# Performance work log

Hardware: AMD Instinct MI355X
Metric: run time of the kernel (lower is better)

The kernel has to match this reference:

```python
import jax, jax.numpy as jnp
import numpy as np

H = 1024
E = 8
TOP_K = 2
B, S = 4, 2048


def setup_inputs() -> dict:
    key = jax.random.key(0)
    ks = jax.random.split(key, 8)
    scale = 0.02
    return {
        "x": jax.random.normal(ks[0], (B, S, H), dtype=jnp.float32),
        "router_w": jax.random.normal(ks[1], (H, E), dtype=jnp.float32) * scale,
        "router_b": jnp.zeros((E,), dtype=jnp.float32),
        "w1": jax.random.normal(ks[2], (E, H, 4 * H), dtype=jnp.float32) * scale,
        "b1": jnp.zeros((E, 4 * H), dtype=jnp.float32),
        "w2": jax.random.normal(ks[3], (E, 4 * H, H), dtype=jnp.float32) * scale,
        "b2": jnp.zeros((E, H), dtype=jnp.float32),
    }


def reference(x, router_w, router_b, w1, b1, w2, b2):
    b, s, h = x.shape
    n_exp = w1.shape[0]
    x_flat = x.reshape(-1, h)  # [T, H]
    T = x_flat.shape[0]

    # Router: softmax then top-k, renormalize top-k probs (matches torch code).
    logits = x_flat @ router_w + router_b            # [T, E]
    probs = jax.nn.softmax(logits, axis=-1)
    top_values, top_indices = jax.lax.top_k(probs, TOP_K)  # [T, k]
    top_values = top_values / jnp.sum(top_values, axis=-1, keepdims=True)

    # Per-token combine weight for each expert (0 if token not routed there).
    combine = jnp.zeros((T, n_exp), dtype=x.dtype)
    combine = combine.at[jnp.arange(T)[:, None], top_indices].add(top_values)  # [T, E]

    # Loop over the small fixed expert set; masked combine weights zero out
    # contributions from unrouted tokens, matching the gather/scatter original.
    out = jnp.zeros_like(x_flat)
    for e in range(n_exp):
        hmid = jax.nn.gelu(x_flat @ w1[e] + b1[e], approximate=False)  # [T, 4H]
        y = hmid @ w2[e] + b2[e]                                       # [T, H]
        out = out + combine[:, e:e + 1] * y
    return out.reshape(b, s, h)
```

## Files before the change

### kernel.cpp

```cpp
#include <hip/hip_runtime.h>
#include <hip/hip_bf16.h>
#include <math.h>

#define TT 8192
#define HD 1024
#define FHD 4096
#define NE 8
#define NTMAX 136

typedef short s16x8 __attribute__((ext_vector_type(8)));
typedef float f32x4 __attribute__((ext_vector_type(4)));
using bf16 = __hip_bfloat16;
typedef unsigned int u32;

#define OFF_COUNTS 0
#define OFF_CURSOR 64
#define OFF_OFFS   128
#define OFF_E0     256
#define OFF_E1     (OFF_E0 + 4*TT)
#define OFF_W0     (OFF_E1 + 4*TT)
#define OFF_W1     (OFF_W0 + 4*TT)
#define OFF_S0     (OFF_W1 + 4*TT)
#define OFF_S1     (OFF_S0 + 4*TT)
#define OFF_TID    (OFF_S1 + 4*TT)
#define OFF_TW     (OFF_TID + 8*TT)
#define OFF_TMR    (OFF_TW + 8*TT)
#define OFF_TME    (OFF_TMR + 4*144)
#define OFF_TMN    (OFF_TME + 4*144)
#define OFF_XBF    (OFF_TMN + 64)
#define OFF_W1T    (OFF_XBF + 2*TT*HD)
#define OFF_W2T    (OFF_W1T + 2*NE*HD*FHD)
#define OFF_HMID   (OFF_W2T + 2*NE*HD*FHD)
#define OFF_YS     (OFF_HMID + (size_t)2*(2*TT)*FHD)

#define BM 128
#define BN 128
#define BK 32

__device__ __forceinline__ void gload_lds16(const void* g, void* l) {
    __builtin_amdgcn_global_load_lds(
        (const __attribute__((address_space(1))) u32*)g,
        (__attribute__((address_space(3))) u32*)l, 16, 0, 0);
}

__global__ __launch_bounds__(256) void cast_x_kernel(const float* __restrict__ x, bf16* __restrict__ xbf) {
    int i = (blockIdx.x * 256 + threadIdx.x) * 8;
    float4 a = *reinterpret_cast<const float4*>(&x[i]);
    float4 b = *reinterpret_cast<const float4*>(&x[i + 4]);
    bf16 h[8];
    h[0] = __float2bfloat16(a.x); h[1] = __float2bfloat16(a.y);
    h[2] = __float2bfloat16(a.z); h[3] = __float2bfloat16(a.w);
    h[4] = __float2bfloat16(b.x); h[5] = __float2bfloat16(b.y);
    h[6] = __float2bfloat16(b.z); h[7] = __float2bfloat16(b.w);
    *reinterpret_cast<uint4*>(&xbf[i]) = *reinterpret_cast<uint4*>(h);
}

__global__ __launch_bounds__(256) void transpose_cast_kernel(const float* __restrict__ in,
        bf16* __restrict__ out, int R, int C) {
    __shared__ float tile[64][65];
    int rt = R >> 6, ct = C >> 6;
    int e = blockIdx.x / (rt * ct);
    int rem = blockIdx.x % (rt * ct);
    int r0 = (rem / ct) << 6, c0 = (rem % ct) << 6;
    const float* ine = in + (size_t)e * R * C;
    bf16* oute = out + (size_t)e * R * C;
    int tid = threadIdx.x;
#pragma unroll
    for (int i = 0; i < 4; ++i) {
        int lin = tid + i * 256;
        int r = lin >> 4, cg = lin & 15;
        float4 v = *reinterpret_cast<const float4*>(&ine[(size_t)(r0 + r) * C + c0 + cg * 4]);
        tile[r][cg * 4 + 0] = v.x; tile[r][cg * 4 + 1] = v.y;
        tile[r][cg * 4 + 2] = v.z; tile[r][cg * 4 + 3] = v.w;
    }
    __syncthreads();
#pragma unroll
    for (int i = 0; i < 4; ++i) {
        int lin = tid + i * 256;
        int n = lin >> 4, kg = lin & 15;
        bf16 h[4];
        h[0] = __float2bfloat16(tile[kg * 4 + 0][n]);
        h[1] = __float2bfloat16(tile[kg * 4 + 1][n]);
        h[2] = __float2bfloat16(tile[kg * 4 + 2][n]);
        h[3] = __float2bfloat16(tile[kg * 4 + 3][n]);
        *reinterpret_cast<uint2*>(&oute[(size_t)(c0 + n) * R + r0 + kg * 4]) =
            *reinterpret_cast<uint2*>(h);
    }
}

__global__ __launch_bounds__(256) void router_kernel(const float* __restrict__ x,
        const float* __restrict__ rw, const float* __restrict__ rb,
        int* __restrict__ e0a, int* __restrict__ e1a,
        float* __restrict__ w0a, float* __restrict__ w1a, int* __restrict__ counts) {
    int wid = threadIdx.x >> 6, lane = threadIdx.x & 63;
    int t = blockIdx.x * 4 + wid;
    const float* xp = x + (size_t)t * HD + lane * 16;
    float xv[16];
#pragma unroll
    for (int j = 0; j < 4; ++j) {
        float4 v = *reinterpret_cast<const float4*>(&xp[j * 4]);
        xv[4 * j] = v.x; xv[4 * j + 1] = v.y; xv[4 * j + 2] = v.z; xv[4 * j + 3] = v.w;
    }
    float acc[8] = {0.f, 0.f, 0.f, 0.f, 0.f, 0.f, 0.f, 0.f};
    const float* rp = rw + (size_t)(lane * 16) * NE;
#pragma unroll
    for (int hh = 0; hh < 16; ++hh) {
        float4 r0 = *reinterpret_cast<const float4*>(&rp[hh * 8]);
        float4 r1 = *reinterpret_cast<const float4*>(&rp[hh * 8 + 4]);
        acc[0] += xv[hh] * r0.x; acc[1] += xv[hh] * r0.y;
        acc[2] += xv[hh] * r0.z; acc[3] += xv[hh] * r0.w;
        acc[4] += xv[hh] * r1.x; acc[5] += xv[hh] * r1.y;
        acc[6] += xv[hh] * r1.z; acc[7] += xv[hh] * r1.w;
    }
#pragma unroll
    for (int e = 0; e < 8; ++e) {
#pragma unroll
        for (int off = 32; off > 0; off >>= 1) acc[e] += __shfl_xor(acc[e], off, 64);
    }
    if (lane == 0) {
        float lg[8];
#pragma unroll
        for (int e = 0; e < 8; ++e) lg[e] = acc[e] + rb[e];
        int a = 0;
#pragma unroll
        for (int e = 1; e < 8; ++e) if (lg[e] > lg[a]) a = e;
        int b = (a == 0) ? 1 : 0;
#pragma unroll
        for (int e = 0; e < 8; ++e) if (e != a && e != b && lg[e] > lg[b]) b = e;
        float wa = 1.0f / (1.0f + expf(lg[b] - lg[a]));
        float wb = 1.0f / (1.0f + expf(lg[a] - lg[b]));
        e0a[t] = a; e1a[t] = b; w0a[t] = wa; w1a[t] = wb;
        atomicAdd(&counts[a], 1);
        atomicAdd(&counts[b], 1);
    }
}

__global__ void scan_offsets_kernel(const int* __restrict__ counts, int* __restrict__ offs,
        int* __restrict__ cursor, int* __restrict__ tmr, int* __restrict__ tme,
        int* __restrict__ tmn) {
    if (threadIdx.x == 0 && blockIdx.x == 0) {
        int s = 0, nt = 0;
        for (int e = 0; e < NE; ++e) {
            offs[e] = s; cursor[e] = s;
            int c = counts[e];
            for (int j = 0; j < c; j += BM) { tmr[nt] = s + j; tme[nt] = e; ++nt; }
            s += c;
        }
        offs[NE] = s;
        tmn[0] = nt;
        for (int i = nt; i < NTMAX; ++i) { tmr[i] = 0; tme[i] = 0; }
    }
}

__global__ __launch_bounds__(256) void scatter_kernel(const int* __restrict__ e0a, const int* __restrict__ e1a,
        const float* __restrict__ w0a, const float* __restrict__ w1a,
        int* __restrict__ cursor, int* __restrict__ tid_arr, float* __restrict__ tw_arr,
        int* __restrict__ slot0, int* __restrict__ slot1) {
    int t = blockIdx.x * 256 + threadIdx.x;
    int s0 = atomicAdd(&cursor[e0a[t]], 1);
    tid_arr[s0] = t; tw_arr[s0] = w0a[t]; slot0[t] = s0;
    int s1 = atomicAdd(&cursor[e1a[t]], 1);
    tid_arr[s1] = t; tw_arr[s1] = w1a[t]; slot1[t] = s1;
}

__global__ __launch_bounds__(256) void gemm1_kernel(const bf16* __restrict__ xbf, const bf16* __restrict__ w1t,
        const float* __restrict__ b1, const int* __restrict__ offs,
        const int* __restrict__ tid_arr, bf16* __restrict__ hmid,
        const int* __restrict__ tmr, const int* __restrict__ tme, const int* __restrict__ tmn) {
    __shared__ bf16 As[BM * BK];
    __shared__ bf16 Bs[BN * BK];
    __shared__ int toks[BM];
    int nwg = gridDim.x;
    int orig = blockIdx.x;
    int wg = (orig & 7) * (nwg >> 3) + (orig >> 3);
    int nt = wg / NTMAX;
    int tidx = wg % NTMAX;
    if (tidx >= tmn[0]) return;
    int e = tme[tidx];
    int row0 = tmr[tidx];
    int s1 = offs[e + 1];
    int n0 = nt * BN;
    int tid = threadIdx.x;
    if (tid < BM) { int s = row0 + tid; toks[tid] = tid_arr[(s < s1) ? s : (s1 - 1)]; }
    __syncthreads();
    int lane = tid & 63, w = tid >> 6;
    int wrow = (w >> 1) * 64, wcol = (w & 1) * 64;
    int lr = lane & 15, lk = (lane >> 4) * 8;
    int srow = lane >> 2, seg = lane & 3;
    int tokA0 = toks[w * 32 + srow];
    int tokA1 = toks[w * 32 + 16 + srow];
    const bf16* w1e = w1t + (size_t)e * FHD * HD;
    const bf16* bsrc0 = w1e + (size_t)(n0 + w * 32 + srow) * HD + seg * 8;
    const bf16* bsrc1 = w1e + (size_t)(n0 + w * 32 + 16 + srow) * HD + seg * 8;
    const bf16* asrc0 = xbf + (size_t)tokA0 * HD + seg * 8;
    const bf16* asrc1 = xbf + (size_t)tokA1 * HD + seg * 8;
    bf16* aDst0 = &As[(w * 32) * BK];
    bf16* aDst1 = &As[(w * 32 + 16) * BK];
    bf16* bDst0 = &Bs[(w * 32) * BK];
    bf16* bDst1 = &Bs[(w * 32 + 16) * BK];
    f32x4 acc[4][4] = {};
    for (int k0 = 0; k0 < HD; k0 += BK) {
        gload_lds16(asrc0 + k0, aDst0);
        gload_lds16(asrc1 + k0, aDst1);
        gload_lds16(bsrc0 + k0, bDst0);
        gload_lds16(bsrc1 + k0, bDst1);
        __syncthreads();
        s16x8 aF[4], bF[4];
#pragma unroll
        for (int m = 0; m < 4; ++m) aF[m] = *reinterpret_cast<const s16x8*>(&As[(wrow + m * 16 + lr) * BK + lk]);
#pragma unroll
        for (int n = 0; n < 4; ++n) bF[n] = *reinterpret_cast<const s16x8*>(&Bs[(wcol + n * 16 + lr) * BK + lk]);
#pragma unroll
        for (int m = 0; m < 4; ++m)
#pragma unroll
            for (int n = 0; n < 4; ++n)
                acc[m][n] = __builtin_amdgcn_mfma_f32_16x16x32_bf16(aF[m], bF[n], acc[m][n], 0, 0, 0);
        __syncthreads();
    }
#pragma unroll
    for (int m = 0; m < 4; ++m) {
#pragma unroll
        for (int n = 0; n < 4; ++n) {
            int col = n0 + wcol + n * 16 + lr;
            float bv = b1[(size_t)e * FHD + col];
#pragma unroll
            for (int r = 0; r < 4; ++r) {
                int row = wrow + m * 16 + (lane >> 4) * 4 + r;
                int slot = row0 + row;
                if (slot < s1) {
                    float v2 = acc[m][n][r] + bv;
                    v2 = 0.5f * v2 * (1.0f + erff(v2 * 0.70710678118f));
                    hmid[(size_t)slot * FHD + col] = __float2bfloat16(v2);
                }
            }
        }
    }
}

__global__ __launch_bounds__(256) void gemm2_kernel(const bf16* __restrict__ hmid, const bf16* __restrict__ w2t,
        const float* __restrict__ b2, const int* __restrict__ offs, float* __restrict__ ys,
        const int* __restrict__ tmr, const int* __restrict__ tme, const int* __restrict__ tmn) {
    __shared__ bf16 As[BM * BK];
    __shared__ bf16 Bs[BN * BK];
    int nwg = gridDim.x;
    int orig = blockIdx.x;
    int wg = (orig & 7) * (nwg >> 3) + (orig >> 3);
    int nt = wg / NTMAX;
    int tidx = wg % NTMAX;
    if (tidx >= tmn[0]) return;
    int e = tme[tidx];
    int row0 = tmr[tidx];
    int s1 = offs[e + 1];
    int n0 = nt * BN;
    int tid = threadIdx.x;
    int lane = tid & 63, w = tid >> 6;
    int wrow = (w >> 1) * 64, wcol = (w & 1) * 64;
    int lr = lane & 15, lk = (lane >> 4) * 8;
    int srow = lane >> 2, seg = lane & 3;
    int ar0 = row0 + w * 32 + srow;      if (ar0 >= s1) ar0 = s1 - 1;
    int ar1 = row0 + w * 32 + 16 + srow; if (ar1 >= s1) ar1 = s1 - 1;
    const bf16* w2e = w2t + (size_t)e * HD * FHD;
    const bf16* bsrc0 = w2e + (size_t)(n0 + w * 32 + srow) * FHD + seg * 8;
    const bf16* bsrc1 = w2e + (size_t)(n0 + w * 32 + 16 + srow) * FHD + seg * 8;
    const bf16* asrc0 = hmid + (size_t)ar0 * FHD + seg * 8;
    const bf16* asrc1 = hmid + (size_t)ar1 * FHD + seg * 8;
    bf16* aDst0 = &As[(w * 32) * BK];
    bf16* aDst1 = &As[(w * 32 + 16) * BK];
    bf16* bDst0 = &Bs[(w * 32) * BK];
    bf16* bDst1 = &Bs[(w * 32 + 16) * BK];
    f32x4 acc[4][4] = {};
    for (int k0 = 0; k0 < FHD; k0 += BK) {
        gload_lds16(asrc0 + k0, aDst0);
        gload_lds16(asrc1 + k0, aDst1);
        gload_lds16(bsrc0 + k0, bDst0);
        gload_lds16(bsrc1 + k0, bDst1);
        __syncthreads();
        s16x8 aF[4], bF[4];
#pragma unroll
        for (int m = 0; m < 4; ++m) aF[m] = *reinterpret_cast<const s16x8*>(&As[(wrow + m * 16 + lr) * BK + lk]);
#pragma unroll
        for (int n = 0; n < 4; ++n) bF[n] = *reinterpret_cast<const s16x8*>(&Bs[(wcol + n * 16 + lr) * BK + lk]);
#pragma unroll
        for (int m = 0; m < 4; ++m)
#pragma unroll
            for (int n = 0; n < 4; ++n)
                acc[m][n] = __builtin_amdgcn_mfma_f32_16x16x32_bf16(aF[m], bF[n], acc[m][n], 0, 0, 0);
        __syncthreads();
    }
#pragma unroll
    for (int m = 0; m < 4; ++m) {
#pragma unroll
        for (int n = 0; n < 4; ++n) {
            int col = n0 + wcol + n * 16 + lr;
            float bv = b2[(size_t)e * HD + col];
#pragma unroll
            for (int r = 0; r < 4; ++r) {
                int row = wrow + m * 16 + (lane >> 4) * 4 + r;
                int slot = row0 + row;
                if (slot < s1) ys[(size_t)slot * HD + col] = acc[m][n][r] + bv;
            }
        }
    }
}

__global__ __launch_bounds__(256) void combine_kernel(const float* __restrict__ ys,
        const int* __restrict__ slot0, const int* __restrict__ slot1,
        const float* __restrict__ tw, float* __restrict__ out) {
    int t = blockIdx.x;
    int c = threadIdx.x * 4;
    int sa = slot0[t], sb = slot1[t];
    float wa = tw[sa], wb = tw[sb];
    float4 a = *reinterpret_cast<const float4*>(&ys[(size_t)sa * HD + c]);
    float4 b = *reinterpret_cast<const float4*>(&ys[(size_t)sb * HD + c]);
    float4 o;
    o.x = wa * a.x + wb * b.x; o.y = wa * a.y + wb * b.y;
    o.z = wa * a.z + wb * b.z; o.w = wa * a.w + wb * b.w;
    *reinterpret_cast<float4*>(&out[(size_t)t * HD + c]) = o;
}

extern "C" void kernel_launch(void* const* d_in, const int* in_sizes, int n_in,
                              void* d_out, int out_size, void* d_ws, size_t ws_size,
                              hipStream_t stream) {
    const float* x  = (const float*)d_in[0];
    const float* rw = (const float*)d_in[1];
    const float* rb = (const float*)d_in[2];
    const float* w1 = (const float*)d_in[3];
    const float* b1 = (const float*)d_in[4];
    const float* w2 = (const float*)d_in[5];
    const float* b2 = (const float*)d_in[6];
    float* out = (float*)d_out;
    char* ws = (char*)d_ws;

    int*   counts  = (int*)(ws + OFF_COUNTS);
    int*   cursor  = (int*)(ws + OFF_CURSOR);
    int*   offs    = (int*)(ws + OFF_OFFS);
    int*   e0a     = (int*)(ws + OFF_E0);
    int*   e1a     = (int*)(ws + OFF_E1);
    float* w0a     = (float*)(ws + OFF_W0);
    float* w1a     = (float*)(ws + OFF_W1);
    int*   slot0   = (int*)(ws + OFF_S0);
    int*   slot1   = (int*)(ws + OFF_S1);
    int*   tid_arr = (int*)(ws + OFF_TID);
    float* tw_arr  = (float*)(ws + OFF_TW);
    int*   tmr     = (int*)(ws + OFF_TMR);
    int*   tme     = (int*)(ws + OFF_TME);
    int*   tmn     = (int*)(ws + OFF_TMN);
    bf16*  xbf     = (bf16*)(ws + OFF_XBF);
    bf16*  w1t     = (bf16*)(ws + OFF_W1T);
    bf16*  w2t     = (bf16*)(ws + OFF_W2T);
    bf16*  hmid    = (bf16*)(ws + OFF_HMID);
    float* ys      = (float*)(ws + OFF_YS);

    hipMemsetAsync(counts, 0, 64, stream);

    cast_x_kernel<<<TT * HD / 2048, 256, 0, stream>>>(x, xbf);
    transpose_cast_kernel<<<NE * (HD / 64) * (FHD / 64), 256, 0, stream>>>(w1, w1t, HD, FHD);
    transpose_cast_kernel<<<NE * (FHD / 64) * (HD / 64), 256, 0, stream>>>(w2, w2t, FHD, HD);
    router_kernel<<<TT / 4, 256, 0, stream>>>(x, rw, rb, e0a, e1a, w0a, w1a, counts);
    scan_offsets_kernel<<<1, 64, 0, stream>>>(counts, offs, cursor, tmr, tme, tmn);
    scatter_kernel<<<TT / 256, 256, 0, stream>>>(e0a, e1a, w0a, w1a, cursor, tid_arr, tw_arr, slot0, slot1);
    gemm1_kernel<<<(FHD / BN) * NTMAX, 256, 0, stream>>>(xbf, w1t, b1, offs, tid_arr, hmid, tmr, tme, tmn);
    gemm2_kernel<<<(HD / BN) * NTMAX, 256, 0, stream>>>(hmid, w2t, b2, offs, ys, tmr, tme, tmn);
    combine_kernel<<<TT, 256, 0, stream>>>(ys, slot0, slot1, tw_arr, out);
}
```

Baseline: 929.2 us.

## Enlarge MoE GEMM tiles, add 4-stage LDS pipeline with swizzled layout

Both expert GEMMs move to 512-thread blocks with 256-row token tiles (256x256 tiles for gemm1, 256x128 for gemm2). The single-buffered LDS loop with two syncthreads per k-step becomes a 4-deep ring buffer that prefetches 3 k-tiles ahead and uses partial vmcnt waits. An XOR swizzle on LDS rows is meant to avoid bank conflicts, and s_setprio is raised around the MFMA block. This targets global-load latency and barrier stalls at the cost of much larger LDS use (128KB in gemm1), lower occupancy, and more padded rows per expert tile.

```diff
diff --git a/kernel.cpp b/kernel.cpp
--- a/kernel.cpp
+++ b/kernel.cpp
@@ -6,7 +6,7 @@
 #define HD 1024
 #define FHD 4096
 #define NE 8
-#define NTMAX 136
+#define TMAX 72
 
 typedef short s16x8 __attribute__((ext_vector_type(8)));
 typedef float f32x4 __attribute__((ext_vector_type(4)));
@@ -33,10 +33,6 @@
 #define OFF_HMID   (OFF_W2T + 2*NE*HD*FHD)
 #define OFF_YS     (OFF_HMID + (size_t)2*(2*TT)*FHD)
 
-#define BM 128
-#define BN 128
-#define BK 32
-
 __device__ __forceinline__ void gload_lds16(const void* g, void* l) {
     __builtin_amdgcn_global_load_lds(
         (const __attribute__((address_space(1))) u32*)g,
@@ -143,12 +139,12 @@
         for (int e = 0; e < NE; ++e) {
             offs[e] = s; cursor[e] = s;
             int c = counts[e];
-            for (int j = 0; j < c; j += BM) { tmr[nt] = s + j; tme[nt] = e; ++nt; }
+            for (int j = 0; j < c; j += 256) { tmr[nt] = s + j; tme[nt] = e; ++nt; }
             s += c;
         }
         offs[NE] = s;
         tmn[0] = nt;
-        for (int i = nt; i < NTMAX; ++i) { tmr[i] = 0; tme[i] = 0; }
+        for (int i = nt; i < TMAX; ++i) { tmr[i] = 0; tme[i] = 0; }
     }
 }
 
@@ -163,69 +159,87 @@
     tid_arr[s1] = t; tw_arr[s1] = w1a[t]; slot1[t] = s1;
 }
 
-__global__ __launch_bounds__(256) void gemm1_kernel(const bf16* __restrict__ xbf, const bf16* __restrict__ w1t,
+__global__ __launch_bounds__(512) void gemm1_kernel(const bf16* __restrict__ xbf, const bf16* __restrict__ w1t,
         const float* __restrict__ b1, const int* __restrict__ offs,
         const int* __restrict__ tid_arr, bf16* __restrict__ hmid,
         const int* __restrict__ tmr, const int* __restrict__ tme, const int* __restrict__ tmn) {
-    __shared__ bf16 As[BM * BK];
-    __shared__ bf16 Bs[BN * BK];
-    __shared__ int toks[BM];
+    __shared__ bf16 As[4 * 256 * 32];
+    __shared__ bf16 Bs[4 * 256 * 32];
+    __shared__ int toks[256];
     int nwg = gridDim.x;
     int orig = blockIdx.x;
     int wg = (orig & 7) * (nwg >> 3) + (orig >> 3);
-    int nt = wg / NTMAX;
-    int tidx = wg % NTMAX;
+    int nt = wg / TMAX, tidx = wg % TMAX;
     if (tidx >= tmn[0]) return;
-    int e = tme[tidx];
-    int row0 = tmr[tidx];
-    int s1 = offs[e + 1];
-    int n0 = nt * BN;
-    int tid = threadIdx.x;
-    if (tid < BM) { int s = row0 + tid; toks[tid] = tid_arr[(s < s1) ? s : (s1 - 1)]; }
+    int e = tme[tidx], row0 = tmr[tidx], s1 = offs[e + 1];
+    int n0 = nt * 256;
+    int t = threadIdx.x;
+    if (t < 256) { int s = row0 + t; toks[t] = tid_arr[(s < s1) ? s : (s1 - 1)]; }
     __syncthreads();
-    int lane = tid & 63, w = tid >> 6;
-    int wrow = (w >> 1) * 64, wcol = (w & 1) * 64;
+    int lane = t & 63, w = t >> 6;
+    const bf16* w1e = w1t + (size_t)e * FHD * HD;
+    int rs = t >> 2, g = t & 3;
+    int swz = (g ^ ((rs >> 1) & 3)) * 8;
+    const bf16* srcA0 = xbf + (size_t)toks[rs] * HD + swz;
+    const bf16* srcA1 = xbf + (size_t)toks[rs + 128] * HD + swz;
+    const bf16* srcB0 = w1e + (size_t)(n0 + rs) * HD + swz;
+    const bf16* srcB1 = w1e + (size_t)(n0 + rs + 128) * HD + swz;
+    int dst0 = w * 512;
+    int dst1 = 4096 + w * 512;
+    int wr = w >> 2, wc = w & 3;
     int lr = lane & 15, lk = (lane >> 4) * 8;
-    int srow = lane >> 2, seg = lane & 3;
-    int tokA0 = toks[w * 32 + srow];
-    int tokA1 = toks[w * 32 + 16 + srow];
-    const bf16* w1e = w1t + (size_t)e * FHD * HD;
-    const bf16* bsrc0 = w1e + (size_t)(n0 + w * 32 + srow) * HD + seg * 8;
-    const bf16* bsrc1 = w1e + (size_t)(n0 + w * 32 + 16 + srow) * HD + seg * 8;
-    const bf16* asrc0 = xbf + (size_t)tokA0 * HD + seg * 8;
-    const bf16* asrc1 = xbf + (size_t)tokA1 * HD + seg * 8;
-    bf16* aDst0 = &As[(w * 32) * BK];
-    bf16* aDst1 = &As[(w * 32 + 16) * BK];
-    bf16* bDst0 = &Bs[(w * 32) * BK];
-    bf16* bDst1 = &Bs[(w * 32 + 16) * BK];
-    f32x4 acc[4][4] = {};
-    for (int k0 = 0; k0 < HD; k0 += BK) {
-        gload_lds16(asrc0 + k0, aDst0);
-        gload_lds16(asrc1 + k0, aDst1);
-        gload_lds16(bsrc0 + k0, bDst0);
-        gload_lds16(bsrc1 + k0, bDst1);
-        __syncthreads();
-        s16x8 aF[4], bF[4];
-#pragma unroll
-        for (int m = 0; m < 4; ++m) aF[m] = *reinterpret_cast<const s16x8*>(&As[(wrow + m * 16 + lr) * BK + lk]);
-#pragma unroll
-        for (int n = 0; n < 4; ++n) bF[n] = *reinterpret_cast<const s16x8*>(&Bs[(wcol + n * 16 + lr) * BK + lk]);
-#pragma unroll
-        for (int m = 0; m < 4; ++m)
+    int offA[8], offB[4];
+#pragma unroll
+    for (int m = 0; m < 8; ++m) { int row = wr * 128 + m * 16 + lr; offA[m] = row * 32 + (lk ^ (8 * ((row >> 1) & 3))); }
+#pragma unroll
+    for (int n = 0; n < 4; ++n) { int row = wc * 64 + n * 16 + lr; offB[n] = row * 32 + (lk ^ (8 * ((row >> 1) & 3))); }
+    f32x4 acc[8][4] = {};
+#pragma unroll
+    for (int kt = 0; kt < 3; ++kt) {
+        int bo = kt * 8192, ko = kt * 32;
+        gload_lds16(srcA0 + ko, &As[bo + dst0]);
+        gload_lds16(srcA1 + ko, &As[bo + dst1]);
+        gload_lds16(srcB0 + ko, &Bs[bo + dst0]);
+        gload_lds16(srcB1 + ko, &Bs[bo + dst1]);
+    }
+    asm volatile("s_waitcnt vmcnt(8)" ::: "memory");
+    __builtin_amdgcn_s_barrier();
+    for (int kt = 0; kt < HD / 32; ++kt) {
+        const bf16* Ab = &As[(kt & 3) * 8192];
+        const bf16* Bb = &Bs[(kt & 3) * 8192];
+        s16x8 aF[8], bF[4];
+#pragma unroll
+        for (int m = 0; m < 8; ++m) aF[m] = *reinterpret_cast<const s16x8*>(&Ab[offA[m]]);
+#pragma unroll
+        for (int n = 0; n < 4; ++n) bF[n] = *reinterpret_cast<const s16x8*>(&Bb[offB[n]]);
+        int kt3 = kt + 3; if (kt3 >= HD / 32) kt3 -= HD / 32;
+        int bo = (kt3 & 3) * 8192, ko = kt3 * 32;
+        gload_lds16(srcA0 + ko, &As[bo + dst0]);
+        gload_lds16(srcA1 + ko, &As[bo + dst1]);
+        gload_lds16(srcB0 + ko, &Bs[bo + dst0]);
+        gload_lds16(srcB1 + ko, &Bs[bo + dst1]);
+        asm volatile("s_waitcnt vmcnt(8)" ::: "memory");
+        __builtin_amdgcn_s_barrier();
+        __builtin_amdgcn_sched_barrier(0);
+        __builtin_amdgcn_s_setprio(1);
+#pragma unroll
+        for (int m = 0; m < 8; ++m)
 #pragma unroll
             for (int n = 0; n < 4; ++n)
                 acc[m][n] = __builtin_amdgcn_mfma_f32_16x16x32_bf16(aF[m], bF[n], acc[m][n], 0, 0, 0);
-        __syncthreads();
-    }
-#pragma unroll
-    for (int m = 0; m < 4; ++m) {
-#pragma unroll
-        for (int n = 0; n < 4; ++n) {
-            int col = n0 + wcol + n * 16 + lr;
-            float bv = b1[(size_t)e * FHD + col];
+        __builtin_amdgcn_s_setprio(0);
+        __builtin_amdgcn_sched_barrier(0);
+        __builtin_amdgcn_s_barrier();
+    }
+#pragma unroll
+    for (int n = 0; n < 4; ++n) {
+        int col = n0 + wc * 64 + n * 16 + lr;
+        float bv = b1[(size_t)e * FHD + col];
+#pragma unroll
+        for (int m = 0; m < 8; ++m) {
 #pragma unroll
             for (int r = 0; r < 4; ++r) {
-                int row = wrow + m * 16 + (lane >> 4) * 4 + r;
+                int row = wr * 128 + m * 16 + (lane >> 4) * 4 + r;
                 int slot = row0 + row;
                 if (slot < s1) {
                     float v2 = acc[m][n][r] + bv;
@@ -237,65 +251,83 @@
     }
 }
 
-__global__ __launch_bounds__(256) void gemm2_kernel(const bf16* __restrict__ hmid, const bf16* __restrict__ w2t,
+__global__ __launch_bounds__(512) void gemm2_kernel(const bf16* __restrict__ hmid, const bf16* __restrict__ w2t,
         const float* __restrict__ b2, const int* __restrict__ offs, float* __restrict__ ys,
         const int* __restrict__ tmr, const int* __restrict__ tme, const int* __restrict__ tmn) {
-    __shared__ bf16 As[BM * BK];
-    __shared__ bf16 Bs[BN * BK];
+    __shared__ bf16 As[4 * 256 * 32];
+    __shared__ bf16 Bs[4 * 128 * 32];
     int nwg = gridDim.x;
     int orig = blockIdx.x;
     int wg = (orig & 7) * (nwg >> 3) + (orig >> 3);
-    int nt = wg / NTMAX;
-    int tidx = wg % NTMAX;
+    int nt = wg / TMAX, tidx = wg % TMAX;
     if (tidx >= tmn[0]) return;
-    int e = tme[tidx];
-    int row0 = tmr[tidx];
-    int s1 = offs[e + 1];
-    int n0 = nt * BN;
-    int tid = threadIdx.x;
-    int lane = tid & 63, w = tid >> 6;
-    int wrow = (w >> 1) * 64, wcol = (w & 1) * 64;
+    int e = tme[tidx], row0 = tmr[tidx], s1 = offs[e + 1];
+    int n0 = nt * 128;
+    int t = threadIdx.x;
+    int lane = t & 63, w = t >> 6;
+    const bf16* w2e = w2t + (size_t)e * HD * FHD;
+    int rs = t >> 2, g = t & 3;
+    int swz = (g ^ ((rs >> 1) & 3)) * 8;
+    int ar0 = row0 + rs;       if (ar0 >= s1) ar0 = s1 - 1;
+    int ar1 = row0 + rs + 128; if (ar1 >= s1) ar1 = s1 - 1;
+    const bf16* srcA0 = hmid + (size_t)ar0 * FHD + swz;
+    const bf16* srcA1 = hmid + (size_t)ar1 * FHD + swz;
+    const bf16* srcB0 = w2e + (size_t)(n0 + rs) * FHD + swz;
+    int dstA0 = w * 512;
+    int dstA1 = 4096 + w * 512;
+    int dstB  = w * 512;
+    int wr = w >> 1, wc = w & 1;
     int lr = lane & 15, lk = (lane >> 4) * 8;
-    int srow = lane >> 2, seg = lane & 3;
-    int ar0 = row0 + w * 32 + srow;      if (ar0 >= s1) ar0 = s1 - 1;
-    int ar1 = row0 + w * 32 + 16 + srow; if (ar1 >= s1) ar1 = s1 - 1;
-    const bf16* w2e = w2t + (size_t)e * HD * FHD;
-    const bf16* bsrc0 = w2e + (size_t)(n0 + w * 32 + srow) * FHD + seg * 8;
-    const bf16* bsrc1 = w2e + (size_t)(n0 + w * 32 + 16 + srow) * FHD + seg * 8;
-    const bf16* asrc0 = hmid + (size_t)ar0 * FHD + seg * 8;
-    const bf16* asrc1 = hmid + (size_t)ar1 * FHD + seg * 8;
-    bf16* aDst0 = &As[(w * 32) * BK];
-    bf16* aDst1 = &As[(w * 32 + 16) * BK];
-    bf16* bDst0 = &Bs[(w * 32) * BK];
-    bf16* bDst1 = &Bs[(w * 32 + 16) * BK];
+    int offA[4], offB[4];
+#pragma unroll
+    for (int m = 0; m < 4; ++m) { int row = wr * 64 + m * 16 + lr; offA[m] = row * 32 + (lk ^ (8 * ((row >> 1) & 3))); }
+#pragma unroll
+    for (int n = 0; n < 4; ++n) { int row = wc * 64 + n * 16 + lr; offB[n] = row * 32 + (lk ^ (8 * ((row >> 1) & 3))); }
     f32x4 acc[4][4] = {};
-    for (int k0 = 0; k0 < FHD; k0 += BK) {
-        gload_lds16(asrc0 + k0, aDst0);
-        gload_lds16(asrc1 + k0, aDst1);
-        gload_lds16(bsrc0 + k0, bDst0);
-        gload_lds16(bsrc1 + k0, bDst1);
-        __syncthreads();
+#pragma unroll
+    for (int kt = 0; kt < 3; ++kt) {
+        int boA = kt * 8192, boB = kt * 4096, ko = kt * 32;
+        gload_lds16(srcA0 + ko, &As[boA + dstA0]);
+        gload_lds16(srcA1 + ko, &As[boA + dstA1]);
+        gload_lds16(srcB0 + ko, &Bs[boB + dstB]);
+    }
+    asm volatile("s_waitcnt vmcnt(6)" ::: "memory");
+    __builtin_amdgcn_s_barrier();
+    for (int kt = 0; kt < FHD / 32; ++kt) {
+        const bf16* Ab = &As[(kt & 3) * 8192];
+        const bf16* Bb = &Bs[(kt & 3) * 4096];
         s16x8 aF[4], bF[4];
 #pragma unroll
-        for (int m = 0; m < 4; ++m) aF[m] = *reinterpret_cast<const s16x8*>(&As[(wrow + m * 16 + lr) * BK + lk]);
-#pragma unroll
-        for (int n = 0; n < 4; ++n) bF[n] = *reinterpret_cast<const s16x8*>(&Bs[(wcol + n * 16 + lr) * BK + lk]);
+        for (int m = 0; m < 4; ++m) aF[m] = *reinterpret_cast<const s16x8*>(&Ab[offA[m]]);
+#pragma unroll
+        for (int n = 0; n < 4; ++n) bF[n] = *reinterpret_cast<const s16x8*>(&Bb[offB[n]]);
+        int kt3 = kt + 3; if (kt3 >= FHD / 32) kt3 -= FHD / 32;
+        int boA = (kt3 & 3) * 8192, boB = (kt3 & 3) * 4096, ko = kt3 * 32;
+        gload_lds16(srcA0 + ko, &As[boA + dstA0]);
+        gload_lds16(srcA1 + ko, &As[boA + dstA1]);
+        gload_lds16(srcB0 + ko, &Bs[boB + dstB]);
+        asm volatile("s_waitcnt vmcnt(6)" ::: "memory");
+        __builtin_amdgcn_s_barrier();
+        __builtin_amdgcn_sched_barrier(0);
+        __builtin_amdgcn_s_setprio(1);
 #pragma unroll
         for (int m = 0; m < 4; ++m)
 #pragma unroll
             for (int n = 0; n < 4; ++n)
                 acc[m][n] = __builtin_amdgcn_mfma_f32_16x16x32_bf16(aF[m], bF[n], acc[m][n], 0, 0, 0);
-        __syncthreads();
-    }
-#pragma unroll
-    for (int m = 0; m < 4; ++m) {
-#pragma unroll
-        for (int n = 0; n < 4; ++n) {
-            int col = n0 + wcol + n * 16 + lr;
-            float bv = b2[(size_t)e * HD + col];
+        __builtin_amdgcn_s_setprio(0);
+        __builtin_amdgcn_sched_barrier(0);
+        __builtin_amdgcn_s_barrier();
+    }
+#pragma unroll
+    for (int n = 0; n < 4; ++n) {
+        int col = n0 + wc * 64 + n * 16 + lr;
+        float bv = b2[(size_t)e * HD + col];
+#pragma unroll
+        for (int m = 0; m < 4; ++m) {
 #pragma unroll
             for (int r = 0; r < 4; ++r) {
-                int row = wrow + m * 16 + (lane >> 4) * 4 + r;
+                int row = wr * 64 + m * 16 + (lane >> 4) * 4 + r;
                 int slot = row0 + row;
                 if (slot < s1) ys[(size_t)slot * HD + col] = acc[m][n][r] + bv;
             }
@@ -359,7 +391,7 @@
     router_kernel<<<TT / 4, 256, 0, stream>>>(x, rw, rb, e0a, e1a, w0a, w1a, counts);
     scan_offsets_kernel<<<1, 64, 0, stream>>>(counts, offs, cursor, tmr, tme, tmn);
     scatter_kernel<<<TT / 256, 256, 0, stream>>>(e0a, e1a, w0a, w1a, cursor, tid_arr, tw_arr, slot0, slot1);
-    gemm1_kernel<<<(FHD / BN) * NTMAX, 256, 0, stream>>>(xbf, w1t, b1, offs, tid_arr, hmid, tmr, tme, tmn);
-    gemm2_kernel<<<(HD / BN) * NTMAX, 256, 0, stream>>>(hmid, w2t, b2, offs, ys, tmr, tme, tmn);
+    gemm1_kernel<<<(FHD / 256) * TMAX, 512, 0, stream>>>(xbf, w1t, b1, offs, tid_arr, hmid, tmr, tme, tmn);
+    gemm2_kernel<<<(HD / 128) * TMAX, 512, 0, stream>>>(hmid, w2t, b2, offs, ys, tmr, tme, tmn);
     combine_kernel<<<TT, 256, 0, stream>>>(ys, slot0, slot1, tw_arr, out);
 }
```

After: 968.9 us. 1.04x slower.

## Widen GEMM K-tile to 64 with swizzled LDS and fuse combine via atomics

Applied to the files above, without the earlier changes.

Both expert GEMMs now load 64-wide K tiles into XOR-swizzled shared memory, which halves the number of barriers per K and is meant to avoid LDS bank conflicts. They also raise MFMA issue priority and set launch bounds for occupancy. The second GEMM applies the routing weight and atomically adds into the zeroed output, which removes the fp32 intermediate buffer and the separate combine kernel. In exchange, the fp32 atomics make the summation order nondeterministic and add atomic traffic to the output.

```diff
diff --git a/kernel.cpp b/kernel.cpp
--- a/kernel.cpp
+++ b/kernel.cpp
@@ -31,11 +31,6 @@
 #define OFF_W1T    (OFF_XBF + 2*TT*HD)
 #define OFF_W2T    (OFF_W1T + 2*NE*HD*FHD)
 #define OFF_HMID   (OFF_W2T + 2*NE*HD*FHD)
-#define OFF_YS     (OFF_HMID + (size_t)2*(2*TT)*FHD)
-
-#define BM 128
-#define BN 128
-#define BK 32
 
 __device__ __forceinline__ void gload_lds16(const void* g, void* l) {
     __builtin_amdgcn_global_load_lds(
@@ -143,7 +138,7 @@
         for (int e = 0; e < NE; ++e) {
             offs[e] = s; cursor[e] = s;
             int c = counts[e];
-            for (int j = 0; j < c; j += BM) { tmr[nt] = s + j; tme[nt] = e; ++nt; }
+            for (int j = 0; j < c; j += 128) { tmr[nt] = s + j; tme[nt] = e; ++nt; }
             s += c;
         }
         offs[NE] = s;
@@ -154,78 +149,94 @@
 
 __global__ __launch_bounds__(256) void scatter_kernel(const int* __restrict__ e0a, const int* __restrict__ e1a,
         const float* __restrict__ w0a, const float* __restrict__ w1a,
-        int* __restrict__ cursor, int* __restrict__ tid_arr, float* __restrict__ tw_arr,
-        int* __restrict__ slot0, int* __restrict__ slot1) {
+        int* __restrict__ cursor, int* __restrict__ tid_arr, float* __restrict__ tw_arr) {
     int t = blockIdx.x * 256 + threadIdx.x;
     int s0 = atomicAdd(&cursor[e0a[t]], 1);
-    tid_arr[s0] = t; tw_arr[s0] = w0a[t]; slot0[t] = s0;
+    tid_arr[s0] = t; tw_arr[s0] = w0a[t];
     int s1 = atomicAdd(&cursor[e1a[t]], 1);
-    tid_arr[s1] = t; tw_arr[s1] = w1a[t]; slot1[t] = s1;
-}
-
-__global__ __launch_bounds__(256) void gemm1_kernel(const bf16* __restrict__ xbf, const bf16* __restrict__ w1t,
-        const float* __restrict__ b1, const int* __restrict__ offs,
-        const int* __restrict__ tid_arr, bf16* __restrict__ hmid,
-        const int* __restrict__ tmr, const int* __restrict__ tme, const int* __restrict__ tmn) {
-    __shared__ bf16 As[BM * BK];
-    __shared__ bf16 Bs[BN * BK];
-    __shared__ int toks[BM];
+    tid_arr[s1] = t; tw_arr[s1] = w1a[t];
+}
+
+__global__ __launch_bounds__(256, 4) void gemm1_kernel(const bf16* __restrict__ xbf,
+        const bf16* __restrict__ w1t, const float* __restrict__ b1,
+        const int* __restrict__ offs, const int* __restrict__ tid_arr,
+        bf16* __restrict__ hmid, const int* __restrict__ tmr,
+        const int* __restrict__ tme, const int* __restrict__ tmn) {
+    __shared__ bf16 As[128 * 64];
+    __shared__ bf16 Bs[128 * 64];
+    __shared__ int toks[128];
     int nwg = gridDim.x;
     int orig = blockIdx.x;
     int wg = (orig & 7) * (nwg >> 3) + (orig >> 3);
-    int nt = wg / NTMAX;
-    int tidx = wg % NTMAX;
+    int nt = wg / NTMAX, tidx = wg % NTMAX;
     if (tidx >= tmn[0]) return;
-    int e = tme[tidx];
-    int row0 = tmr[tidx];
-    int s1 = offs[e + 1];
-    int n0 = nt * BN;
-    int tid = threadIdx.x;
-    if (tid < BM) { int s = row0 + tid; toks[tid] = tid_arr[(s < s1) ? s : (s1 - 1)]; }
+    int e = tme[tidx], row0 = tmr[tidx], s1 = offs[e + 1];
+    int n0 = nt * 128;
+    int t = threadIdx.x;
+    if (t < 128) { int s = row0 + t; toks[t] = tid_arr[(s < s1) ? s : (s1 - 1)]; }
     __syncthreads();
-    int lane = tid & 63, w = tid >> 6;
-    int wrow = (w >> 1) * 64, wcol = (w & 1) * 64;
-    int lr = lane & 15, lk = (lane >> 4) * 8;
-    int srow = lane >> 2, seg = lane & 3;
-    int tokA0 = toks[w * 32 + srow];
-    int tokA1 = toks[w * 32 + 16 + srow];
+    int lane = t & 63, w = t >> 6;
+    int wr = w >> 1, wc = w & 1;
+    int lr = lane & 15, kg = lane >> 4;
+    int srow = t >> 3, soct = t & 7;
+    int socts = (soct ^ (srow & 7)) * 8;
     const bf16* w1e = w1t + (size_t)e * FHD * HD;
-    const bf16* bsrc0 = w1e + (size_t)(n0 + w * 32 + srow) * HD + seg * 8;
-    const bf16* bsrc1 = w1e + (size_t)(n0 + w * 32 + 16 + srow) * HD + seg * 8;
-    const bf16* asrc0 = xbf + (size_t)tokA0 * HD + seg * 8;
-    const bf16* asrc1 = xbf + (size_t)tokA1 * HD + seg * 8;
-    bf16* aDst0 = &As[(w * 32) * BK];
-    bf16* aDst1 = &As[(w * 32 + 16) * BK];
-    bf16* bDst0 = &Bs[(w * 32) * BK];
-    bf16* bDst1 = &Bs[(w * 32 + 16) * BK];
+    const bf16* pA[4]; const bf16* pB[4];
+#pragma unroll
+    for (int i = 0; i < 4; ++i) {
+        int r = i * 32 + srow;
+        pA[i] = xbf + (size_t)toks[r] * HD + socts;
+        pB[i] = w1e + (size_t)(n0 + r) * HD + socts;
+    }
+    int ldst = t * 8;
+    int offA[4][2], offB[4][2];
+#pragma unroll
+    for (int m = 0; m < 4; ++m) {
+        int rowA = wr * 64 + m * 16 + lr;
+        int rowB = wc * 64 + m * 16 + lr;
+#pragma unroll
+        for (int ks = 0; ks < 2; ++ks) {
+            offA[m][ks] = rowA * 64 + ((ks * 32 + kg * 8) ^ ((lr & 7) << 3));
+            offB[m][ks] = rowB * 64 + ((ks * 32 + kg * 8) ^ ((lr & 7) << 3));
+        }
+    }
     f32x4 acc[4][4] = {};
-    for (int k0 = 0; k0 < HD; k0 += BK) {
-        gload_lds16(asrc0 + k0, aDst0);
-        gload_lds16(asrc1 + k0, aDst1);
-        gload_lds16(bsrc0 + k0, bDst0);
-        gload_lds16(bsrc1 + k0, bDst1);
+    for (int kt = 0; kt < HD / 64; ++kt) {
+        int ko = kt * 64;
+#pragma unroll
+        for (int i = 0; i < 4; ++i) {
+            gload_lds16(pA[i] + ko, &As[i * 2048 + ldst]);
+            gload_lds16(pB[i] + ko, &Bs[i * 2048 + ldst]);
+        }
         __syncthreads();
-        s16x8 aF[4], bF[4];
-#pragma unroll
-        for (int m = 0; m < 4; ++m) aF[m] = *reinterpret_cast<const s16x8*>(&As[(wrow + m * 16 + lr) * BK + lk]);
-#pragma unroll
-        for (int n = 0; n < 4; ++n) bF[n] = *reinterpret_cast<const s16x8*>(&Bs[(wcol + n * 16 + lr) * BK + lk]);
+        s16x8 af[4][2], bfr[4][2];
 #pragma unroll
         for (int m = 0; m < 4; ++m)
 #pragma unroll
+            for (int ks = 0; ks < 2; ++ks) {
+                af[m][ks] = *reinterpret_cast<const s16x8*>(&As[offA[m][ks]]);
+                bfr[m][ks] = *reinterpret_cast<const s16x8*>(&Bs[offB[m][ks]]);
+            }
+        __builtin_amdgcn_s_setprio(1);
+#pragma unroll
+        for (int m = 0; m < 4; ++m)
+#pragma unroll
             for (int n = 0; n < 4; ++n)
-                acc[m][n] = __builtin_amdgcn_mfma_f32_16x16x32_bf16(aF[m], bF[n], acc[m][n], 0, 0, 0);
+#pragma unroll
+                for (int ks = 0; ks < 2; ++ks)
+                    acc[m][n] = __builtin_amdgcn_mfma_f32_16x16x32_bf16(af[m][ks], bfr[n][ks], acc[m][n], 0, 0, 0);
+        __builtin_amdgcn_s_setprio(0);
         __syncthreads();
     }
 #pragma unroll
     for (int m = 0; m < 4; ++m) {
 #pragma unroll
         for (int n = 0; n < 4; ++n) {
-            int col = n0 + wcol + n * 16 + lr;
+            int col = n0 + wc * 64 + n * 16 + lr;
             float bv = b1[(size_t)e * FHD + col];
 #pragma unroll
             for (int r = 0; r < 4; ++r) {
-                int row = wrow + m * 16 + (lane >> 4) * 4 + r;
+                int row = wr * 64 + m * 16 + kg * 4 + r;
                 int slot = row0 + row;
                 if (slot < s1) {
                     float v2 = acc[m][n][r] + bv;
@@ -237,85 +248,101 @@
     }
 }
 
-__global__ __launch_bounds__(256) void gemm2_kernel(const bf16* __restrict__ hmid, const bf16* __restrict__ w2t,
-        const float* __restrict__ b2, const int* __restrict__ offs, float* __restrict__ ys,
+__global__ __launch_bounds__(256, 4) void gemm2_kernel(const bf16* __restrict__ hmid,
+        const bf16* __restrict__ w2t, const float* __restrict__ b2,
+        const int* __restrict__ offs, const int* __restrict__ tid_arr,
+        const float* __restrict__ tw_arr, float* __restrict__ out,
         const int* __restrict__ tmr, const int* __restrict__ tme, const int* __restrict__ tmn) {
-    __shared__ bf16 As[BM * BK];
-    __shared__ bf16 Bs[BN * BK];
+    __shared__ bf16 As[128 * 64];
+    __shared__ bf16 Bs[128 * 64];
+    __shared__ int toks[128];
+    __shared__ float tws[128];
     int nwg = gridDim.x;
     int orig = blockIdx.x;
     int wg = (orig & 7) * (nwg >> 3) + (orig >> 3);
-    int nt = wg / NTMAX;
-    int tidx = wg % NTMAX;
+    int nt = wg / NTMAX, tidx = wg % NTMAX;
     if (tidx >= tmn[0]) return;
-    int e = tme[tidx];
-    int row0 = tmr[tidx];
-    int s1 = offs[e + 1];
-    int n0 = nt * BN;
-    int tid = threadIdx.x;
-    int lane = tid & 63, w = tid >> 6;
-    int wrow = (w >> 1) * 64, wcol = (w & 1) * 64;
-    int lr = lane & 15, lk = (lane >> 4) * 8;
-    int srow = lane >> 2, seg = lane & 3;
-    int ar0 = row0 + w * 32 + srow;      if (ar0 >= s1) ar0 = s1 - 1;
-    int ar1 = row0 + w * 32 + 16 + srow; if (ar1 >= s1) ar1 = s1 - 1;
+    int e = tme[tidx], row0 = tmr[tidx], s1 = offs[e + 1];
+    int n0 = nt * 128;
+    int t = threadIdx.x;
+    if (t < 128) {
+        int s = row0 + t;
+        int sc = (s < s1) ? s : (s1 - 1);
+        toks[t] = tid_arr[sc];
+        tws[t] = tw_arr[sc];
+    }
+    __syncthreads();
+    int lane = t & 63, w = t >> 6;
+    int wr = w >> 1, wc = w & 1;
+    int lr = lane & 15, kg = lane >> 4;
+    int srow = t >> 3, soct = t & 7;
+    int socts = (soct ^ (srow & 7)) * 8;
     const bf16* w2e = w2t + (size_t)e * HD * FHD;
-    const bf16* bsrc0 = w2e + (size_t)(n0 + w * 32 + srow) * FHD + seg * 8;
-    const bf16* bsrc1 = w2e + (size_t)(n0 + w * 32 + 16 + srow) * FHD + seg * 8;
-    const bf16* asrc0 = hmid + (size_t)ar0 * FHD + seg * 8;
-    const bf16* asrc1 = hmid + (size_t)ar1 * FHD + seg * 8;
-    bf16* aDst0 = &As[(w * 32) * BK];
-    bf16* aDst1 = &As[(w * 32 + 16) * BK];
-    bf16* bDst0 = &Bs[(w * 32) * BK];
-    bf16* bDst1 = &Bs[(w * 32 + 16) * BK];
+    const bf16* pA[4]; const bf16* pB[4];
+#pragma unroll
+    for (int i = 0; i < 4; ++i) {
+        int r = i * 32 + srow;
+        int ar = row0 + r; if (ar >= s1) ar = s1 - 1;
+        pA[i] = hmid + (size_t)ar * FHD + socts;
+        pB[i] = w2e + (size_t)(n0 + r) * FHD + socts;
+    }
+    int ldst = t * 8;
+    int offA[4][2], offB[4][2];
+#pragma unroll
+    for (int m = 0; m < 4; ++m) {
+        int rowA = wr * 64 + m * 16 + lr;
+        int rowB = wc * 64 + m * 16 + lr;
+#pragma unroll
+        for (int ks = 0; ks < 2; ++ks) {
+            offA[m][ks] = rowA * 64 + ((ks * 32 + kg * 8) ^ ((lr & 7) << 3));
+            offB[m][ks] = rowB * 64 + ((ks * 32 + kg * 8) ^ ((lr & 7) << 3));
+        }
+    }
     f32x4 acc[4][4] = {};
-    for (int k0 = 0; k0 < FHD; k0 += BK) {
-        gload_lds16(asrc0 + k0, aDst0);
-        gload_lds16(asrc1 + k0, aDst1);
-        gload_lds16(bsrc0 + k0, bDst0);
-        gload_lds16(bsrc1 + k0, bDst1);
+    for (int kt = 0; kt < FHD / 64; ++kt) {
+        int ko = kt * 64;
+#pragma unroll
+        for (int i = 0; i < 4; ++i) {
+            gload_lds16(pA[i] + ko, &As[i * 2048 + ldst]);
+            gload_lds16(pB[i] + ko, &Bs[i * 2048 + ldst]);
+        }
         __syncthreads();
-        s16x8 aF[4], bF[4];
-#pragma unroll
-        for (int m = 0; m < 4; ++m) aF[m] = *reinterpret_cast<const s16x8*>(&As[(wrow + m * 16 + lr) * BK + lk]);
-#pragma unroll
-        for (int n = 0; n < 4; ++n) bF[n] = *reinterpret_cast<const s16x8*>(&Bs[(wcol + n * 16 + lr) * BK + lk]);
+        s16x8 af[4][2], bfr[4][2];
 #pragma unroll
         for (int m = 0; m < 4; ++m)
 #pragma unroll
+            for (int ks = 0; ks < 2; ++ks) {
+                af[m][ks] = *reinterpret_cast<const s16x8*>(&As[offA[m][ks]]);
+                bfr[m][ks] = *reinterpret_cast<const s16x8*>(&Bs[offB[m][ks]]);
+            }
+        __builtin_amdgcn_s_setprio(1);
+#pragma unroll
+        for (int m = 0; m < 4; ++m)
+#pragma unroll
             for (int n = 0; n < 4; ++n)
-                acc[m][n] = __builtin_amdgcn_mfma_f32_16x16x32_bf16(aF[m], bF[n], acc[m][n], 0, 0, 0);
+#pragma unroll
+                for (int ks = 0; ks < 2; ++ks)
+                    acc[m][n] = __builtin_amdgcn_mfma_f32_16x16x32_bf16(af[m][ks], bfr[n][ks], acc[m][n], 0, 0, 0);
+        __builtin_amdgcn_s_setprio(0);
         __syncthreads();
     }
 #pragma unroll
     for (int m = 0; m < 4; ++m) {
 #pragma unroll
         for (int n = 0; n < 4; ++n) {
-            int col = n0 + wcol + n * 16 + lr;
+            int col = n0 + wc * 64 + n * 16 + lr;
             float bv = b2[(size_t)e * HD + col];
 #pragma unroll
             for (int r = 0; r < 4; ++r) {
-                int row = wrow + m * 16 + (lane >> 4) * 4 + r;
+                int row = wr * 64 + m * 16 + kg * 4 + r;
                 int slot = row0 + row;
-                if (slot < s1) ys[(size_t)slot * HD + col] = acc[m][n][r] + bv;
+                if (slot < s1) {
+                    float val = tws[row] * (acc[m][n][r] + bv);
+                    atomicAdd(&out[(size_t)toks[row] * HD + col], val);
+                }
             }
         }
     }
-}
-
-__global__ __launch_bounds__(256) void combine_kernel(const float* __restrict__ ys,
-        const int* __restrict__ slot0, const int* __restrict__ slot1,
-        const float* __restrict__ tw, float* __restrict__ out) {
-    int t = blockIdx.x;
-    int c = threadIdx.x * 4;
-    int sa = slot0[t], sb = slot1[t];
-    float wa = tw[sa], wb = tw[sb];
-    float4 a = *reinterpret_cast<const float4*>(&ys[(size_t)sa * HD + c]);
-    float4 b = *reinterpret_cast<const float4*>(&ys[(size_t)sb * HD + c]);
-    float4 o;
-    o.x = wa * a.x + wb * b.x; o.y = wa * a.y + wb * b.y;
-    o.z = wa * a.z + wb * b.z; o.w = wa * a.w + wb * b.w;
-    *reinterpret_cast<float4*>(&out[(size_t)t * HD + c]) = o;
 }
 
 extern "C" void kernel_launch(void* const* d_in, const int* in_sizes, int n_in,
@@ -338,8 +365,6 @@
     int*   e1a     = (int*)(ws + OFF_E1);
     float* w0a     = (float*)(ws + OFF_W0);
     float* w1a     = (float*)(ws + OFF_W1);
-    int*   slot0   = (int*)(ws + OFF_S0);
-    int*   slot1   = (int*)(ws + OFF_S1);
     int*   tid_arr = (int*)(ws + OFF_TID);
     float* tw_arr  = (float*)(ws + OFF_TW);
     int*   tmr     = (int*)(ws + OFF_TMR);
@@ -349,17 +374,16 @@
     bf16*  w1t     = (bf16*)(ws + OFF_W1T);
     bf16*  w2t     = (bf16*)(ws + OFF_W2T);
     bf16*  hmid    = (bf16*)(ws + OFF_HMID);
-    float* ys      = (float*)(ws + OFF_YS);
 
     hipMemsetAsync(counts, 0, 64, stream);
+    hipMemsetAsync(out, 0, (size_t)TT * HD * sizeof(float), stream);
 
     cast_x_kernel<<<TT * HD / 2048, 256, 0, stream>>>(x, xbf);
     transpose_cast_kernel<<<NE * (HD / 64) * (FHD / 64), 256, 0, stream>>>(w1, w1t, HD, FHD);
     transpose_cast_kernel<<<NE * (FHD / 64) * (HD / 64), 256, 0, stream>>>(w2, w2t, FHD, HD);
     router_kernel<<<TT / 4, 256, 0, stream>>>(x, rw, rb, e0a, e1a, w0a, w1a, counts);
     scan_offsets_kernel<<<1, 64, 0, stream>>>(counts, offs, cursor, tmr, tme, tmn);
-    scatter_kernel<<<TT / 256, 256, 0, stream>>>(e0a, e1a, w0a, w1a, cursor, tid_arr, tw_arr, slot0, slot1);
-    gemm1_kernel<<<(FHD / BN) * NTMAX, 256, 0, stream>>>(xbf, w1t, b1, offs, tid_arr, hmid, tmr, tme, tmn);
-    gemm2_kernel<<<(HD / BN) * NTMAX, 256, 0, stream>>>(hmid, w2t, b2, offs, ys, tmr, tme, tmn);
-    combine_kernel<<<TT, 256, 0, stream>>>(ys, slot0, slot1, tw_arr, out);
-}
+    scatter_kernel<<<TT / 256, 256, 0, stream>>>(e0a, e1a, w0a, w1a, cursor, tid_arr, tw_arr);
+    gemm1_kernel<<<(FHD / 128) * NTMAX, 256, 0, stream>>>(xbf, w1t, b1, offs, tid_arr, hmid, tmr, tme, tmn);
+    gemm2_kernel<<<(HD / 128) * NTMAX, 256, 0, stream>>>(hmid, w2t, b2, offs, tid_arr, tw_arr, out, tmr, tme, tmn);
+}
```

Measured after the change: 1.669 ms. +79.6%, slower.
